# Kernel tuning notes

Hardware: AMD Instinct MI355X
Metric: run time of the kernel (lower is better)

## Reference

```python
import jax, jax.numpy as jnp
import numpy as np

B, S, D, H = 4, 1024, 512, 8
DH = D // H  # dim_head = 64
LN_EPS = 1e-5
COS_EPS = 1e-8


def setup_inputs() -> dict:
    key = jax.random.key(0)
    ks = jax.random.split(key, 8)
    q = jax.random.normal(ks[0], (B, S, D), dtype=jnp.float32)
    k = jax.random.normal(ks[1], (B, S, D), dtype=jnp.float32)
    v = jax.random.normal(ks[2], (B, S, D), dtype=jnp.float32)
    ln_g = jnp.ones((D,), jnp.float32)
    ln_b = jnp.zeros((D,), jnp.float32)
    W_in = jax.random.normal(ks[3], (D, D), dtype=jnp.float32) / np.sqrt(D)
    W_out = jax.random.normal(ks[4], (D, D), dtype=jnp.float32) / np.sqrt(D)
    b_out = jnp.zeros((D,), jnp.float32)
    cov_w = jnp.float32(0.6)
    var_w = jnp.float32(0.2)
    return {"q": q, "k": k, "v": v, "ln_g": ln_g, "ln_b": ln_b,
            "W_in": W_in, "W_out": W_out, "b_out": b_out,
            "cov_w": cov_w, "var_w": var_w}


def reference(q, k, v, ln_g, ln_b, W_in, W_out, b_out, cov_w, var_w):
    def transform(x):
        # input_layernorm followed by bias-free input_linear
        mu = jnp.mean(x, axis=-1, keepdims=True)
        var = jnp.var(x, axis=-1, keepdims=True)
        xn = (x - mu) * jax.lax.rsqrt(var + LN_EPS) * ln_g + ln_b
        y = xn @ W_in
        # 'q n (h d) -> h q n d'
        return y.reshape(B, S, H, DH).transpose(2, 0, 1, 3)

    f_q = transform(q)  # [h, b, n, d]
    f_k = transform(k)  # [h, b, m, d]
    f_v = transform(v)  # [h, b, m, d]

    # cosine_distance(f_q, f_k^T)
    dots = jnp.einsum('hbnd,hbmd->hbnm', f_q, f_k)
    qn = jnp.linalg.norm(f_q, axis=-1)  # [h, b, n]
    kn = jnp.linalg.norm(f_k, axis=-1)  # [h, b, m]
    cosine_sim = dots / (qn[..., :, None] * kn[..., None, :] + COS_EPS)

    # basic_attention_components
    q_c = f_q - jnp.mean(f_q, axis=-1, keepdims=True)
    k_c = f_k - jnp.mean(f_k, axis=-1, keepdims=True)
    cov_component = jnp.einsum('hbnd,hbmd->hbnm', q_c, k_c) / DH
    q_var = jnp.var(f_q, axis=-1, ddof=1)  # torch.var unbiased=True
    k_var = jnp.var(f_k, axis=-1, ddof=1)
    var_component = (q_var[..., :, None] * k_var[..., None, :]) / DH

    # fixed learned-scalar mixing (dynamic_weight=False path)
    attn = (cov_w * cov_component + var_w * var_component
            + (1.0 - cov_w - var_w) * cosine_sim)

    out = jnp.einsum('hbnm,hbmd->hbnd', attn, f_v)
    # 'h q n d -> q n (h d)'
    out = out.transpose(1, 2, 0, 3).reshape(B, S, D)
    return out @ W_out + b_out
```

## Files before the change

kernel.cpp:

```cpp
#include <hip/hip_runtime.h>


#define R_TOT 4096
#define DD 512
#define HB_N 32

typedef __attribute__((ext_vector_type(8))) short short8;
typedef __attribute__((ext_vector_type(4))) float f32x4;

static __device__ inline unsigned short f2bf(float f) {
    union { float f; unsigned u; } x{f};
    unsigned r = x.u + 0x7fff + ((x.u >> 16) & 1);
    return (unsigned short)(r >> 16);
}

static __device__ inline unsigned scale2(unsigned u, float a, float b) {
    float lo = __uint_as_float(u << 16);
    float hi = __uint_as_float(u & 0xffff0000u);
    return (unsigned)f2bf(lo * a) | ((unsigned)f2bf(hi * b) << 16);
}

static __device__ inline void async_cp16(const unsigned short* g, unsigned short* l) {
    __builtin_amdgcn_global_load_lds(
        (const __attribute__((address_space(1))) unsigned int*)g,
        (__attribute__((address_space(3))) unsigned int*)l, 16, 0, 0);
}

__global__ __launch_bounds__(256) void k1_ln_prep(
    const float* __restrict__ q, const float* __restrict__ k, const float* __restrict__ v,
    const float* __restrict__ ln_g, const float* __restrict__ ln_b,
    const float* __restrict__ Win, const float* __restrict__ Wout,
    unsigned short* __restrict__ xn, unsigned short* __restrict__ WinT,
    unsigned short* __restrict__ WoutT)
{
    int blk = blockIdx.x;
    int t = threadIdx.x;
    if (blk < 3 * R_TOT) {
        const float* src = (blk < R_TOT) ? q : (blk < 2 * R_TOT ? k : v);
        const float* x = src + (size_t)(blk & (R_TOT - 1)) * DD;
        float2 val = *(const float2*)(x + t * 2);
        float s = val.x + val.y;
        float s2 = val.x * val.x + val.y * val.y;
        #pragma unroll
        for (int o = 32; o; o >>= 1) { s += __shfl_xor(s, o); s2 += __shfl_xor(s2, o); }
        __shared__ float red[8];
        int wv = t >> 6;
        if ((t & 63) == 0) { red[wv] = s; red[4 + wv] = s2; }
        __syncthreads();
        s = red[0] + red[1] + red[2] + red[3];
        s2 = red[4] + red[5] + red[6] + red[7];
        float mu = s * (1.f / 512.f);
        float var = s2 * (1.f / 512.f) - mu * mu;
        float rstd = rsqrtf(var + 1e-5f);
        float2 gg = *(const float2*)(ln_g + t * 2);
        float2 bb = *(const float2*)(ln_b + t * 2);
        unsigned short* o = xn + (size_t)blk * DD + t * 2;
        o[0] = f2bf((val.x - mu) * rstd * gg.x + bb.x);
        o[1] = f2bf((val.y - mu) * rstd * gg.y + bb.y);
    } else {
        __shared__ float tl[64][65];
        int bb = blk - 3 * R_TOT;
        const float* src = (bb & 64) ? Wout : Win;
        unsigned short* dst = (bb & 64) ? WoutT : WinT;
        int tile = bb & 63;
        int r0 = (tile >> 3) * 64, c0 = (tile & 7) * 64;
        #pragma unroll
        for (int rep = 0; rep < 16; rep++) {
            int rr = rep * 4 + (t >> 6), cc = t & 63;
            tl[rr][cc] = src[(size_t)(r0 + rr) * DD + c0 + cc];
        }
        __syncthreads();
        #pragma unroll
        for (int rep = 0; rep < 16; rep++) {
            int rr = rep * 4 + (t >> 6), cc = t & 63;
            dst[(size_t)(c0 + rr) * DD + r0 + cc] = f2bf(tl[cc][rr]);
        }
    }
}

__global__ __launch_bounds__(256) void gemm_qkv(
    const unsigned short* __restrict__ A, const unsigned short* __restrict__ Bt,
    unsigned short* __restrict__ A2, unsigned short* __restrict__ Lt,
    unsigned short* __restrict__ Vt)
{
    __shared__ __align__(16) char smbuf[39936];
    unsigned short* AsF = (unsigned short*)smbuf;
    unsigned short* BsF = (unsigned short*)(smbuf + 16384);
    int t = threadIdx.x, lane = t & 63, wv = t >> 6;
    int quad = lane >> 4, l15 = lane & 15;
    int m0 = blockIdx.y * 128, n0 = blockIdx.x * 128;
    int wr = (wv >> 1) * 64, wc = (wv & 1) * 64;
    int swz = l15 & 7;
    int r8 = lane >> 3, cc8 = lane & 7;
    f32x4 acc[4][4] = {};
    for (int kt = 0; kt < 512; kt += 64) {
        __syncthreads();
        #pragma unroll
        for (int gi = 0; gi < 4; gi++) {
            int grp = wv * 4 + gi;
            int row = grp * 8 + r8;
            int col = kt + ((cc8 ^ (row & 7)) << 3);
            async_cp16(A + (size_t)(m0 + row) * 512 + col, AsF + grp * 512);
            async_cp16(Bt + (size_t)(n0 + row) * 512 + col, BsF + grp * 512);
        }
        __syncthreads();
        #pragma unroll
        for (int kk = 0; kk < 2; kk++) {
            short8 af[4], bf[4];
            int ksl = ((kk * 4 + quad) ^ swz) << 3;
            #pragma unroll
            for (int i = 0; i < 4; i++) af[i] = *(const short8*)&AsF[(wr + i * 16 + l15) * 64 + ksl];
            #pragma unroll
            for (int j = 0; j < 4; j++) bf[j] = *(const short8*)&BsF[(wc + j * 16 + l15) * 64 + ksl];
            #pragma unroll
            for (int i = 0; i < 4; i++)
                #pragma unroll
                for (int j = 0; j < 4; j++)
                    acc[i][j] = __builtin_amdgcn_mfma_f32_16x16x32_bf16(af[i], bf[j], acc[i][j], 0, 0, 0);
        }
    }
    __syncthreads();

    unsigned short* tile = (unsigned short*)(smbuf + wv * 9216);
    float* st     = (float*)(smbuf + 36864 + wv * 768);
    float* st_inv = st;
    float* st_var = st + 64;
    float* st_mu  = st + 128;

    int typ  = m0 >> 12;
    int rloc = (m0 & 4095) + wr;
    int b = rloc >> 10, sb = rloc & 1023;
    int h = (n0 + wc) >> 6;
    int hb = h * 4 + b;

    if (typ < 2) {
        #pragma unroll
        for (int i = 0; i < 4; i++)
            #pragma unroll
            for (int r = 0; r < 4; r++) {
                float a0 = acc[i][0][r], a1 = acc[i][1][r], a2 = acc[i][2][r], a3 = acc[i][3][r];
                float s1 = a0 + a1 + a2 + a3;
                float s2 = a0 * a0 + a1 * a1 + a2 * a2 + a3 * a3;
                #pragma unroll
                for (int o = 1; o < 16; o <<= 1) { s1 += __shfl_xor(s1, o); s2 += __shfl_xor(s2, o); }
                if (l15 == 0) {
                    int sl = i * 16 + quad * 4 + r;
                    float mu = s1 * (1.f / 64.f);
                    st_inv[sl] = rsqrtf(fmaxf(s2, 1e-20f));
                    st_var[sl] = (s2 - 64.f * mu * mu) * (1.f / 63.f);
                    st_mu[sl]  = mu;
                }
            }
    }
    #pragma unroll
    for (int i = 0; i < 4; i++)
        #pragma unroll
        for (int j = 0; j < 4; j++)
            #pragma unroll
            for (int r = 0; r < 4; r++) {
                int sl = i * 16 + quad * 4 + r, d = j * 16 + l15;
                unsigned short bv = f2bf(acc[i][j][r]);
                tile[(typ == 0) ? (sl * 72 + d) : (d * 72 + sl)] = bv;
            }

    if (typ == 0) {
        unsigned short* ob = A2 + ((size_t)hb * 1024 + sb) * 160;
        #pragma unroll
        for (int it = 0; it < 8; it++) {
            int sl = it * 8 + (lane >> 3), ch = (lane & 7) * 8;
            uint4 raw = *(uint4*)&tile[sl * 72 + ch];
            *(uint4*)(ob + (size_t)sl * 160 + ch) = raw;
            float iv = st_inv[sl];
            uint4 o2;
            o2.x = scale2(raw.x, iv, iv); o2.y = scale2(raw.y, iv, iv);
            o2.z = scale2(raw.z, iv, iv); o2.w = scale2(raw.w, iv, iv);
            *(uint4*)(ob + (size_t)sl * 160 + 64 + ch) = o2;
        }
        {
            int sl = lane;
            uint4 z = {0, 0, 0, 0};
            uint4 t0 = z;
            t0.x = (unsigned)f2bf(st_var[sl]) | ((unsigned)f2bf(st_mu[sl]) << 16);
            unsigned short* p = ob + (size_t)sl * 160 + 128;
            *(uint4*)p = t0;
            *(uint4*)(p + 8) = z; *(uint4*)(p + 16) = z; *(uint4*)(p + 24) = z;
        }
    } else if (typ == 1) {
        unsigned short* lb = Lt + (size_t)hb * 160 * 1024 + sb;
        #pragma unroll
        for (int it = 0; it < 8; it++) {
            int d = it * 8 + (lane >> 3), ch = (lane & 7) * 8;
            uint4 raw = *(uint4*)&tile[d * 72 + ch];
            *(uint4*)(lb + (size_t)d * 1024 + ch) = raw;
            const float* ivp = st_inv + ch;
            uint4 o2;
            o2.x = scale2(raw.x, ivp[0], ivp[1]); o2.y = scale2(raw.y, ivp[2], ivp[3]);
            o2.z = scale2(raw.z, ivp[4], ivp[5]); o2.w = scale2(raw.w, ivp[6], ivp[7]);
            *(uint4*)(lb + (size_t)(64 + d) * 1024 + ch) = o2;
        }
        if (lane < 16) {
            int which = lane >> 3, ch = (lane & 7) * 8;
            const float* sp = (which ? st_mu : st_var) + ch;
            uint4 o;
            o.x = (unsigned)f2bf(sp[0]) | ((unsigned)f2bf(sp[1]) << 16);
            o.y = (unsigned)f2bf(sp[2]) | ((unsigned)f2bf(sp[3]) << 16);
            o.z = (unsigned)f2bf(sp[4]) | ((unsigned)f2bf(sp[5]) << 16);
            o.w = (unsigned)f2bf(sp[6]) | ((unsigned)f2bf(sp[7]) << 16);
            *(uint4*)(lb + (size_t)(128 + which) * 1024 + ch) = o;
        }
        uint4 z = {0, 0, 0, 0};
        for (int zi = lane; zi < 240; zi += 64) {
            int d = 130 + (zi >> 3), ch = (zi & 7) * 8;
            *(uint4*)(lb + (size_t)d * 1024 + ch) = z;
        }
    } else {
        unsigned short* vb = Vt + (size_t)hb * 64 * 1024 + sb;
        #pragma unroll
        for (int it = 0; it < 8; it++) {
            int d = it * 8 + (lane >> 3), ch = (lane & 7) * 8;
            uint4 raw = *(uint4*)&tile[d * 72 + ch];
            *(uint4*)(vb + (size_t)d * 1024 + ch) = raw;
        }
    }
}

__global__ __launch_bounds__(256) void gemm512(
    const unsigned short* __restrict__ A, const unsigned short* __restrict__ Bt,
    float* __restrict__ C, const float* __restrict__ bias)
{
    __shared__ __align__(16) unsigned short As[128][40];
    __shared__ __align__(16) unsigned short Bs[128][40];
    int t = threadIdx.x, lane = t & 63, wv = t >> 6;
    int quad = lane >> 4, l15 = lane & 15;
    int m0 = blockIdx.y * 128, n0 = blockIdx.x * 128;
    int wr = (wv >> 1) * 64, wc = (wv & 1) * 64;
    f32x4 acc[4][4] = {};
    for (int kt = 0; kt < 512; kt += 32) {
        __syncthreads();
        #pragma unroll
        for (int ld = 0; ld < 2; ld++) {
            int id = ld * 256 + t;
            int row = id >> 2, co = (id & 3) * 8;
            *(uint4*)&As[row][co] = *(const uint4*)(A + (size_t)(m0 + row) * 512 + kt + co);
            *(uint4*)&Bs[row][co] = *(const uint4*)(Bt + (size_t)(n0 + row) * 512 + kt + co);
        }
        __syncthreads();
        short8 af[4], bf[4];
        #pragma unroll
        for (int i = 0; i < 4; i++) af[i] = *(const short8*)&As[wr + i * 16 + l15][quad * 8];
        #pragma unroll
        for (int j = 0; j < 4; j++) bf[j] = *(const short8*)&Bs[wc + j * 16 + l15][quad * 8];
        #pragma unroll
        for (int i = 0; i < 4; i++)
            #pragma unroll
            for (int j = 0; j < 4; j++)
                acc[i][j] = __builtin_amdgcn_mfma_f32_16x16x32_bf16(af[i], bf[j], acc[i][j], 0, 0, 0);
    }
    #pragma unroll
    for (int i = 0; i < 4; i++)
        #pragma unroll
        for (int j = 0; j < 4; j++)
            #pragma unroll
            for (int r = 0; r < 4; r++) {
                int rr = m0 + wr + i * 16 + quad * 4 + r;
                int cc = n0 + wc + j * 16 + l15;
                float vv = acc[i][j][r];
                if (bias) vv += bias[cc];
                C[(size_t)rr * 512 + cc] = vv;
            }
}

__global__ __launch_bounds__(256) void k4_ktv(
    const unsigned short* __restrict__ Lt, const unsigned short* __restrict__ Vt,
    float* __restrict__ Cpart)
{
    int hb = blockIdx.x, kt = blockIdx.y;
    int t = threadIdx.x, lane = t & 63, wv = t >> 6;
    int quad = lane >> 4, l15 = lane & 15;
    __shared__ __align__(16) unsigned short As[160][72];
    __shared__ __align__(16) unsigned short Bs[64][72];
    const unsigned short* Ab = Lt + (size_t)hb * 160 * 1024 + kt * 128;
    const unsigned short* Bb = Vt + (size_t)hb * 64 * 1024 + kt * 128;
    f32x4 acc[10] = {};
    for (int kc = 0; kc < 128; kc += 64) {
        __syncthreads();
        #pragma unroll
        for (int i = 0; i < 5; i++) {
            int id = i * 256 + t;
            int row = id >> 3, co = (id & 7) * 8;
            *(uint4*)&As[row][co] = *(const uint4*)(Ab + (size_t)row * 1024 + kc + co);
        }
        #pragma unroll
        for (int i = 0; i < 2; i++) {
            int id = i * 256 + t;
            int row = id >> 3, co = (id & 7) * 8;
            *(uint4*)&Bs[row][co] = *(const uint4*)(Bb + (size_t)row * 1024 + kc + co);
        }
        __syncthreads();
        #pragma unroll
        for (int kk = 0; kk < 2; kk++) {
            short8 bfrag = *(const short8*)&Bs[wv * 16 + l15][kk * 32 + quad * 8];
            #pragma unroll
            for (int mt = 0; mt < 10; mt++) {
                short8 afrag = *(const short8*)&As[mt * 16 + l15][kk * 32 + quad * 8];
                acc[mt] = __builtin_amdgcn_mfma_f32_16x16x32_bf16(afrag, bfrag, acc[mt], 0, 0, 0);
            }
        }
    }
    float* ob = Cpart + ((size_t)hb * 8 + kt) * (160 * 64);
    #pragma unroll
    for (int mt = 0; mt < 10; mt++)
        #pragma unroll
        for (int r = 0; r < 4; r++)
            ob[(mt * 16 + quad * 4 + r) * 64 + wv * 16 + l15] = acc[mt][r];
}

__global__ __launch_bounds__(256) void k5_reduce(
    const float* __restrict__ Cpart, unsigned short* __restrict__ B2t,
    const float* __restrict__ covp, const float* __restrict__ varp)
{
    int hb = blockIdx.x, c0 = blockIdx.y * 32, t = threadIdx.x;
    float cov = covp[0], vw = varp[0];
    float c1 = cov * (1.f / 64.f), cw = 1.f - cov - vw;
    float vw64 = vw * (1.f / 64.f), c2 = -cov;
    const float* base = Cpart + (size_t)hb * 8 * 10240;
    unsigned short* ob = B2t + (size_t)hb * 10240;
    #pragma unroll
    for (int rep = 0; rep < 8; rep++) {
        int o = rep * 256 + t;
        int kk = c0 + (o >> 6), d = o & 63;
        float s = 0;
        #pragma unroll
        for (int c = 0; c < 8; c++) s += base[c * 10240 + kk * 64 + d];
        float scale = (kk < 64) ? c1 : (kk < 128) ? cw : (kk == 128) ? vw64 : (kk == 129) ? c2 : 0.f;
        ob[d * 160 + kk] = f2bf(scale * s);
    }
}

__global__ __launch_bounds__(256) void k6_apply(
    const unsigned short* __restrict__ A2, const unsigned short* __restrict__ B2t,
    unsigned short* __restrict__ g)
{
    int hb = blockIdx.y, h = hb >> 2, b = hb & 3;
    int m0 = blockIdx.x * 128;
    int t = threadIdx.x, lane = t & 63, wv = t >> 6;
    int quad = lane >> 4, l15 = lane & 15;
    __shared__ __align__(16) unsigned short As[128][40];
    __shared__ __align__(16) unsigned short Bs[64][40];
    const unsigned short* Ab = A2 + (size_t)hb * 1024 * 160;
    const unsigned short* Bb = B2t + (size_t)hb * 10240;
    f32x4 acc[2][4] = {};
    for (int kt = 0; kt < 160; kt += 32) {
        __syncthreads();
        #pragma unroll
        for (int ld = 0; ld < 2; ld++) {
            int id = ld * 256 + t;
            int row = id >> 2, co = (id & 3) * 8;
            *(uint4*)&As[row][co] = *(const uint4*)(Ab + (size_t)(m0 + row) * 160 + kt + co);
        }
        {
            int row = t >> 2, co = (t & 3) * 8;
            *(uint4*)&Bs[row][co] = *(const uint4*)(Bb + (size_t)row * 160 + kt + co);
        }
        __syncthreads();
        short8 af[2], bf[4];
        #pragma unroll
        for (int i = 0; i < 2; i++) af[i] = *(const short8*)&As[wv * 32 + i * 16 + l15][quad * 8];
        #pragma unroll
        for (int j = 0; j < 4; j++) bf[j] = *(const short8*)&Bs[j * 16 + l15][quad * 8];
        #pragma unroll
        for (int i = 0; i < 2; i++)
            #pragma unroll
            for (int j = 0; j < 4; j++)
                acc[i][j] = __builtin_amdgcn_mfma_f32_16x16x32_bf16(af[i], bf[j], acc[i][j], 0, 0, 0);
    }
    #pragma unroll
    for (int i = 0; i < 2; i++)
        #pragma unroll
        for (int j = 0; j < 4; j++)
            #pragma unroll
            for (int r = 0; r < 4; r++) {
                int rr = m0 + wv * 32 + i * 16 + quad * 4 + r;
                int cc = j * 16 + l15;
                g[((size_t)b * 1024 + rr) * 512 + h * 64 + cc] = f2bf(acc[i][j][r]);
            }
}

extern "C" void kernel_launch(void* const* d_in, const int* in_sizes, int n_in,
                              void* d_out, int out_size, void* d_ws, size_t ws_size,
                              hipStream_t stream)
{
    const float* q    = (const float*)d_in[0];
    const float* k    = (const float*)d_in[1];
    const float* v    = (const float*)d_in[2];
    const float* ln_g = (const float*)d_in[3];
    const float* ln_b = (const float*)d_in[4];
    const float* Win  = (const float*)d_in[5];
    const float* Wout = (const float*)d_in[6];
    const float* bout = (const float*)d_in[7];
    const float* covw = (const float*)d_in[8];
    const float* varw = (const float*)d_in[9];

    char* ws = (char*)d_ws;
    size_t off = 0;
    auto alloc = [&](size_t bytes) { size_t r = off; off += (bytes + 255) & ~(size_t)255; return r; };
    unsigned short* xn    = (unsigned short*)(ws + alloc((size_t)3 * R_TOT * DD * 2));
    unsigned short* WinT  = (unsigned short*)(ws + alloc((size_t)DD * DD * 2));
    unsigned short* WoutT = (unsigned short*)(ws + alloc((size_t)DD * DD * 2));
    unsigned short* A2    = (unsigned short*)(ws + alloc((size_t)HB_N * 1024 * 160 * 2));
    unsigned short* Lt    = (unsigned short*)(ws + alloc((size_t)HB_N * 160 * 1024 * 2));
    unsigned short* Vt    = (unsigned short*)(ws + alloc((size_t)HB_N * 64 * 1024 * 2));
    float*          Cpart = (float*)(ws + alloc((size_t)HB_N * 8 * 10240 * 4));
    unsigned short* g     = (unsigned short*)(ws + alloc((size_t)R_TOT * DD * 2));
    unsigned short* B2t   = (unsigned short*)(ws + alloc((size_t)HB_N * 10240 * 2));
    (void)ws_size; (void)in_sizes; (void)n_in; (void)out_size;

    k1_ln_prep<<<3 * R_TOT + 128, 256, 0, stream>>>(q, k, v, ln_g, ln_b, Win, Wout, xn, WinT, WoutT);
    gemm_qkv<<<dim3(4, 96), 256, 0, stream>>>(xn, WinT, A2, Lt, Vt);
    k4_ktv<<<dim3(HB_N, 8), 256, 0, stream>>>(Lt, Vt, Cpart);
    k5_reduce<<<dim3(HB_N, 5), 256, 0, stream>>>(Cpart, B2t, covw, varw);
    k6_apply<<<dim3(8, HB_N), 256, 0, stream>>>(A2, B2t, g);
    gemm512<<<dim3(4, 32), 256, 0, stream>>>(g, WoutT, (float*)d_out, bout);
}
```

Baseline: 153.7 us.

## Fuse K^T V product with reduction and compute scaled K rows on the fly

The QKV GEMM now writes only raw K plus per-row inv-norm, variance and mean, instead of the full 160-row augmented L matrix. A new per-head-batch kernel builds the scaled and statistics rows in shared memory, runs the whole K^T V product over all 1024 keys, and writes the mixed, scaled B2t directly. This removes the split-K partial buffer and the separate reduce kernel. The output GEMM also uses 128x64 tiles to double the block count. The fused kernel launches only 32 blocks, so it trades lower memory traffic and one fewer launch for much less parallelism in that stage.

```diff
diff --git a/kernel.cpp b/kernel.cpp
--- a/kernel.cpp
+++ b/kernel.cpp
@@ -80,8 +80,9 @@
 
 __global__ __launch_bounds__(256) void gemm_qkv(
     const unsigned short* __restrict__ A, const unsigned short* __restrict__ Bt,
-    unsigned short* __restrict__ A2, unsigned short* __restrict__ Lt,
-    unsigned short* __restrict__ Vt)
+    unsigned short* __restrict__ A2, unsigned short* __restrict__ Kt,
+    unsigned short* __restrict__ Vt, float* __restrict__ kinv,
+    float* __restrict__ kvar, float* __restrict__ kmu)
 {
     __shared__ __align__(16) char smbuf[39936];
     unsigned short* AsF = (unsigned short*)smbuf;
@@ -186,155 +187,109 @@
             *(uint4*)(p + 8) = z; *(uint4*)(p + 16) = z; *(uint4*)(p + 24) = z;
         }
     } else if (typ == 1) {
-        unsigned short* lb = Lt + (size_t)hb * 160 * 1024 + sb;
+        unsigned short* kb = Kt + (size_t)hb * 64 * 1024 + sb;
         #pragma unroll
         for (int it = 0; it < 8; it++) {
             int d = it * 8 + (lane >> 3), ch = (lane & 7) * 8;
             uint4 raw = *(uint4*)&tile[d * 72 + ch];
-            *(uint4*)(lb + (size_t)d * 1024 + ch) = raw;
-            const float* ivp = st_inv + ch;
-            uint4 o2;
-            o2.x = scale2(raw.x, ivp[0], ivp[1]); o2.y = scale2(raw.y, ivp[2], ivp[3]);
-            o2.z = scale2(raw.z, ivp[4], ivp[5]); o2.w = scale2(raw.w, ivp[6], ivp[7]);
-            *(uint4*)(lb + (size_t)(64 + d) * 1024 + ch) = o2;
-        }
-        if (lane < 16) {
-            int which = lane >> 3, ch = (lane & 7) * 8;
-            const float* sp = (which ? st_mu : st_var) + ch;
+            *(uint4*)(kb + (size_t)d * 1024 + ch) = raw;
+        }
+        int mi = hb * 1024 + sb + lane;
+        kinv[mi] = st_inv[lane];
+        kvar[mi] = st_var[lane];
+        kmu[mi]  = st_mu[lane];
+    } else {
+        unsigned short* vb = Vt + (size_t)hb * 64 * 1024 + sb;
+        #pragma unroll
+        for (int it = 0; it < 8; it++) {
+            int d = it * 8 + (lane >> 3), ch = (lane & 7) * 8;
+            uint4 raw = *(uint4*)&tile[d * 72 + ch];
+            *(uint4*)(vb + (size_t)d * 1024 + ch) = raw;
+        }
+    }
+}
+
+__global__ __launch_bounds__(256) void k45_ktv(
+    const unsigned short* __restrict__ Kt, const unsigned short* __restrict__ Vt,
+    const float* __restrict__ kinv, const float* __restrict__ kvar,
+    const float* __restrict__ kmu, unsigned short* __restrict__ B2t,
+    const float* __restrict__ covp, const float* __restrict__ varp)
+{
+    __shared__ __align__(16) unsigned short As[144][136];
+    __shared__ __align__(16) unsigned short Bs[64][136];
+    __shared__ float sinv[128], svar[128], smu[128];
+    int hb = blockIdx.x;
+    int t = threadIdx.x, lane = t & 63, wv = t >> 6;
+    int quad = lane >> 4, l15 = lane & 15;
+    float cov = covp[0], vw = varp[0];
+    float c1 = cov * (1.f / 64.f), cw = 1.f - cov - vw;
+    float vw64 = vw * (1.f / 64.f), c2 = -cov;
+    const unsigned short* Kb = Kt + (size_t)hb * 64 * 1024;
+    const unsigned short* Vb = Vt + (size_t)hb * 64 * 1024;
+    int sbase = hb * 1024;
+    if (t < 224) {
+        int row = 130 + (t >> 4), co = (t & 15) * 8;
+        uint4 z = {0, 0, 0, 0};
+        *(uint4*)&As[row][co] = z;
+    }
+    f32x4 acc[9] = {};
+    for (int kc = 0; kc < 8; kc++) {
+        __syncthreads();
+        if (t < 128) {
+            int m = kc * 128 + t;
+            sinv[t] = kinv[sbase + m]; svar[t] = kvar[sbase + m]; smu[t] = kmu[sbase + m];
+        }
+        uint4 kraw[4];
+        #pragma unroll
+        for (int i = 0; i < 4; i++) {
+            int id = i * 256 + t, row = id >> 4, co = (id & 15) * 8;
+            kraw[i] = *(const uint4*)(Kb + (size_t)row * 1024 + kc * 128 + co);
+            *(uint4*)&As[row][co] = kraw[i];
+            uint4 vr = *(const uint4*)(Vb + (size_t)row * 1024 + kc * 128 + co);
+            *(uint4*)&Bs[row][co] = vr;
+        }
+        __syncthreads();
+        #pragma unroll
+        for (int i = 0; i < 4; i++) {
+            int id = i * 256 + t, row = id >> 4, co = (id & 15) * 8;
+            float4 iva = *(const float4*)&sinv[co];
+            float4 ivb = *(const float4*)&sinv[co + 4];
+            uint4 o;
+            o.x = scale2(kraw[i].x, iva.x, iva.y); o.y = scale2(kraw[i].y, iva.z, iva.w);
+            o.z = scale2(kraw[i].z, ivb.x, ivb.y); o.w = scale2(kraw[i].w, ivb.z, ivb.w);
+            *(uint4*)&As[64 + row][co] = o;
+        }
+        if (t < 32) {
+            int which = t >> 4, j0 = (t & 15) * 8;
+            const float* sp = (which ? smu : svar) + j0;
             uint4 o;
             o.x = (unsigned)f2bf(sp[0]) | ((unsigned)f2bf(sp[1]) << 16);
             o.y = (unsigned)f2bf(sp[2]) | ((unsigned)f2bf(sp[3]) << 16);
             o.z = (unsigned)f2bf(sp[4]) | ((unsigned)f2bf(sp[5]) << 16);
             o.w = (unsigned)f2bf(sp[6]) | ((unsigned)f2bf(sp[7]) << 16);
-            *(uint4*)(lb + (size_t)(128 + which) * 1024 + ch) = o;
-        }
-        uint4 z = {0, 0, 0, 0};
-        for (int zi = lane; zi < 240; zi += 64) {
-            int d = 130 + (zi >> 3), ch = (zi & 7) * 8;
-            *(uint4*)(lb + (size_t)d * 1024 + ch) = z;
-        }
-    } else {
-        unsigned short* vb = Vt + (size_t)hb * 64 * 1024 + sb;
-        #pragma unroll
-        for (int it = 0; it < 8; it++) {
-            int d = it * 8 + (lane >> 3), ch = (lane & 7) * 8;
-            uint4 raw = *(uint4*)&tile[d * 72 + ch];
-            *(uint4*)(vb + (size_t)d * 1024 + ch) = raw;
-        }
-    }
-}
-
-__global__ __launch_bounds__(256) void gemm512(
-    const unsigned short* __restrict__ A, const unsigned short* __restrict__ Bt,
-    float* __restrict__ C, const float* __restrict__ bias)
-{
-    __shared__ __align__(16) unsigned short As[128][40];
-    __shared__ __align__(16) unsigned short Bs[128][40];
-    int t = threadIdx.x, lane = t & 63, wv = t >> 6;
-    int quad = lane >> 4, l15 = lane & 15;
-    int m0 = blockIdx.y * 128, n0 = blockIdx.x * 128;
-    int wr = (wv >> 1) * 64, wc = (wv & 1) * 64;
-    f32x4 acc[4][4] = {};
-    for (int kt = 0; kt < 512; kt += 32) {
-        __syncthreads();
-        #pragma unroll
-        for (int ld = 0; ld < 2; ld++) {
-            int id = ld * 256 + t;
-            int row = id >> 2, co = (id & 3) * 8;
-            *(uint4*)&As[row][co] = *(const uint4*)(A + (size_t)(m0 + row) * 512 + kt + co);
-            *(uint4*)&Bs[row][co] = *(const uint4*)(Bt + (size_t)(n0 + row) * 512 + kt + co);
-        }
-        __syncthreads();
-        short8 af[4], bf[4];
-        #pragma unroll
-        for (int i = 0; i < 4; i++) af[i] = *(const short8*)&As[wr + i * 16 + l15][quad * 8];
-        #pragma unroll
-        for (int j = 0; j < 4; j++) bf[j] = *(const short8*)&Bs[wc + j * 16 + l15][quad * 8];
-        #pragma unroll
-        for (int i = 0; i < 4; i++)
-            #pragma unroll
-            for (int j = 0; j < 4; j++)
-                acc[i][j] = __builtin_amdgcn_mfma_f32_16x16x32_bf16(af[i], bf[j], acc[i][j], 0, 0, 0);
-    }
-    #pragma unroll
-    for (int i = 0; i < 4; i++)
-        #pragma unroll
-        for (int j = 0; j < 4; j++)
-            #pragma unroll
-            for (int r = 0; r < 4; r++) {
-                int rr = m0 + wr + i * 16 + quad * 4 + r;
-                int cc = n0 + wc + j * 16 + l15;
-                float vv = acc[i][j][r];
-                if (bias) vv += bias[cc];
-                C[(size_t)rr * 512 + cc] = vv;
-            }
-}
-
-__global__ __launch_bounds__(256) void k4_ktv(
-    const unsigned short* __restrict__ Lt, const unsigned short* __restrict__ Vt,
-    float* __restrict__ Cpart)
-{
-    int hb = blockIdx.x, kt = blockIdx.y;
-    int t = threadIdx.x, lane = t & 63, wv = t >> 6;
-    int quad = lane >> 4, l15 = lane & 15;
-    __shared__ __align__(16) unsigned short As[160][72];
-    __shared__ __align__(16) unsigned short Bs[64][72];
-    const unsigned short* Ab = Lt + (size_t)hb * 160 * 1024 + kt * 128;
-    const unsigned short* Bb = Vt + (size_t)hb * 64 * 1024 + kt * 128;
-    f32x4 acc[10] = {};
-    for (int kc = 0; kc < 128; kc += 64) {
-        __syncthreads();
-        #pragma unroll
-        for (int i = 0; i < 5; i++) {
-            int id = i * 256 + t;
-            int row = id >> 3, co = (id & 7) * 8;
-            *(uint4*)&As[row][co] = *(const uint4*)(Ab + (size_t)row * 1024 + kc + co);
-        }
-        #pragma unroll
-        for (int i = 0; i < 2; i++) {
-            int id = i * 256 + t;
-            int row = id >> 3, co = (id & 7) * 8;
-            *(uint4*)&Bs[row][co] = *(const uint4*)(Bb + (size_t)row * 1024 + kc + co);
-        }
-        __syncthreads();
-        #pragma unroll
-        for (int kk = 0; kk < 2; kk++) {
+            *(uint4*)&As[128 + which][j0] = o;
+        }
+        __syncthreads();
+        #pragma unroll
+        for (int kk = 0; kk < 4; kk++) {
             short8 bfrag = *(const short8*)&Bs[wv * 16 + l15][kk * 32 + quad * 8];
             #pragma unroll
-            for (int mt = 0; mt < 10; mt++) {
+            for (int mt = 0; mt < 9; mt++) {
                 short8 afrag = *(const short8*)&As[mt * 16 + l15][kk * 32 + quad * 8];
                 acc[mt] = __builtin_amdgcn_mfma_f32_16x16x32_bf16(afrag, bfrag, acc[mt], 0, 0, 0);
             }
         }
     }
-    float* ob = Cpart + ((size_t)hb * 8 + kt) * (160 * 64);
+    unsigned short* ob = B2t + (size_t)hb * 10240;
+    int d = wv * 16 + l15;
     #pragma unroll
-    for (int mt = 0; mt < 10; mt++)
-        #pragma unroll
-        for (int r = 0; r < 4; r++)
-            ob[(mt * 16 + quad * 4 + r) * 64 + wv * 16 + l15] = acc[mt][r];
-}
-
-__global__ __launch_bounds__(256) void k5_reduce(
-    const float* __restrict__ Cpart, unsigned short* __restrict__ B2t,
-    const float* __restrict__ covp, const float* __restrict__ varp)
-{
-    int hb = blockIdx.x, c0 = blockIdx.y * 32, t = threadIdx.x;
-    float cov = covp[0], vw = varp[0];
-    float c1 = cov * (1.f / 64.f), cw = 1.f - cov - vw;
-    float vw64 = vw * (1.f / 64.f), c2 = -cov;
-    const float* base = Cpart + (size_t)hb * 8 * 10240;
-    unsigned short* ob = B2t + (size_t)hb * 10240;
-    #pragma unroll
-    for (int rep = 0; rep < 8; rep++) {
-        int o = rep * 256 + t;
-        int kk = c0 + (o >> 6), d = o & 63;
-        float s = 0;
-        #pragma unroll
-        for (int c = 0; c < 8; c++) s += base[c * 10240 + kk * 64 + d];
-        float scale = (kk < 64) ? c1 : (kk < 128) ? cw : (kk == 128) ? vw64 : (kk == 129) ? c2 : 0.f;
-        ob[d * 160 + kk] = f2bf(scale * s);
-    }
+    for (int mt = 0; mt < 9; mt++)
+        #pragma unroll
+        for (int r = 0; r < 4; r++) {
+            int kk = mt * 16 + quad * 4 + r;
+            float scale = (kk < 64) ? c1 : (kk < 128) ? cw : (kk == 128) ? vw64 : (kk == 129) ? c2 : 0.f;
+            ob[d * 160 + kk] = f2bf(scale * acc[mt][r]);
+        }
 }
 
 __global__ __launch_bounds__(256) void k6_apply(
@@ -386,6 +341,52 @@
             }
 }
 
+__global__ __launch_bounds__(256) void gemm_out(
+    const unsigned short* __restrict__ A, const unsigned short* __restrict__ Bt,
+    float* __restrict__ C, const float* __restrict__ bias)
+{
+    __shared__ __align__(16) unsigned short As[128][40];
+    __shared__ __align__(16) unsigned short Bs[64][40];
+    int t = threadIdx.x, lane = t & 63, wv = t >> 6;
+    int quad = lane >> 4, l15 = lane & 15;
+    int m0 = blockIdx.y * 128, n0 = blockIdx.x * 64;
+    f32x4 acc[2][4] = {};
+    for (int kt = 0; kt < 512; kt += 32) {
+        __syncthreads();
+        #pragma unroll
+        for (int ld = 0; ld < 2; ld++) {
+            int id = ld * 256 + t;
+            int row = id >> 2, co = (id & 3) * 8;
+            *(uint4*)&As[row][co] = *(const uint4*)(A + (size_t)(m0 + row) * 512 + kt + co);
+        }
+        {
+            int row = t >> 2, co = (t & 3) * 8;
+            *(uint4*)&Bs[row][co] = *(const uint4*)(Bt + (size_t)(n0 + row) * 512 + kt + co);
+        }
+        __syncthreads();
+        short8 af[2], bf[4];
+        #pragma unroll
+        for (int i = 0; i < 2; i++) af[i] = *(const short8*)&As[wv * 32 + i * 16 + l15][quad * 8];
+        #pragma unroll
+        for (int j = 0; j < 4; j++) bf[j] = *(const short8*)&Bs[j * 16 + l15][quad * 8];
+        #pragma unroll
+        for (int i = 0; i < 2; i++)
+            #pragma unroll
+            for (int j = 0; j < 4; j++)
+                acc[i][j] = __builtin_amdgcn_mfma_f32_16x16x32_bf16(af[i], bf[j], acc[i][j], 0, 0, 0);
+    }
+    #pragma unroll
+    for (int i = 0; i < 2; i++)
+        #pragma unroll
+        for (int j = 0; j < 4; j++)
+            #pragma unroll
+            for (int r = 0; r < 4; r++) {
+                int rr = m0 + wv * 32 + i * 16 + quad * 4 + r;
+                int cc = n0 + j * 16 + l15;
+                C[(size_t)rr * 512 + cc] = acc[i][j][r] + bias[cc];
+            }
+}
+
 extern "C" void kernel_launch(void* const* d_in, const int* in_sizes, int n_in,
                               void* d_out, int out_size, void* d_ws, size_t ws_size,
                               hipStream_t stream)
@@ -408,17 +409,18 @@
     unsigned short* WinT  = (unsigned short*)(ws + alloc((size_t)DD * DD * 2));
     unsigned short* WoutT = (unsigned short*)(ws + alloc((size_t)DD * DD * 2));
     unsigned short* A2    = (unsigned short*)(ws + alloc((size_t)HB_N * 1024 * 160 * 2));
-    unsigned short* Lt    = (unsigned short*)(ws + alloc((size_t)HB_N * 160 * 1024 * 2));
+    unsigned short* Kt    = (unsigned short*)(ws + alloc((size_t)HB_N * 64 * 1024 * 2));
     unsigned short* Vt    = (unsigned short*)(ws + alloc((size_t)HB_N * 64 * 1024 * 2));
-    float*          Cpart = (float*)(ws + alloc((size_t)HB_N * 8 * 10240 * 4));
+    float*          kinv  = (float*)(ws + alloc((size_t)HB_N * 1024 * 4));
+    float*          kvar  = (float*)(ws + alloc((size_t)HB_N * 1024 * 4));
+    float*          kmu   = (float*)(ws + alloc((size_t)HB_N * 1024 * 4));
     unsigned short* g     = (unsigned short*)(ws + alloc((size_t)R_TOT * DD * 2));
     unsigned short* B2t   = (unsigned short*)(ws + alloc((size_t)HB_N * 10240 * 2));
     (void)ws_size; (void)in_sizes; (void)n_in; (void)out_size;
 
     k1_ln_prep<<<3 * R_TOT + 128, 256, 0, stream>>>(q, k, v, ln_g, ln_b, Win, Wout, xn, WinT, WoutT);
-    gemm_qkv<<<dim3(4, 96), 256, 0, stream>>>(xn, WinT, A2, Lt, Vt);
-    k4_ktv<<<dim3(HB_N, 8), 256, 0, stream>>>(Lt, Vt, Cpart);
-    k5_reduce<<<dim3(HB_N, 5), 256, 0, stream>>>(Cpart, B2t, covw, varw);
+    gemm_qkv<<<dim3(4, 96), 256, 0, stream>>>(xn, WinT, A2, Kt, Vt, kinv, kvar, kmu);
+    k45_ktv<<<HB_N, 256, 0, stream>>>(Kt, Vt, kinv, kvar, kmu, B2t, covw, varw);
     k6_apply<<<dim3(8, HB_N), 256, 0, stream>>>(A2, B2t, g);
-    gemm512<<<dim3(4, 32), 256, 0, stream>>>(g, WoutT, (float*)d_out, bout);
-}
+    gemm_out<<<dim3(8, 32), 256, 0, stream>>>(g, WoutT, (float*)d_out, bout);
+}
```

New measurement: 152.2 us. No clear change (-1.0%).
